# Performance work log

Measured on AMD Instinct MI355X. Metric: run time of the kernel, lower is better.

The kernel has to match this reference:

```python
import jax, jax.numpy as jnp
import numpy as np

# BTT dims for in=out=4096, square mode: m=n=64, a=b=64, rank=8
M, N, A, B_BLK, RANK = 64, 64, 64, 64, 8
OUT_FEATURES = M * A  # 4096


def setup_inputs() -> dict:
    key = jax.random.key(0)
    k_x, k_r, k_l = jax.random.split(key, 3)
    x = jax.random.normal(k_x, (4, 1024, 4096), dtype=jnp.float32)
    # btt_r: (n, b, m*rank); btt_l: (m, rank*n, a)
    btt_r = jax.random.normal(k_r, (N, B_BLK, M * RANK), dtype=jnp.float32) * 0.02
    btt_l = jax.random.normal(k_l, (M, RANK * N, A), dtype=jnp.float32) * 0.02
    bias = jnp.zeros((OUT_FEATURES,), dtype=jnp.float32)
    return {"x": x, "btt_r": btt_r, "btt_l": btt_l, "bias": bias}


def reference(x, btt_r, btt_l, bias):
    n, b, mr = btt_r.shape
    m, rn, a = btt_l.shape
    rank = mr // m
    orig_shape = x.shape
    xr = x.reshape(-1, n, b)          # (B, n, b)
    Bn = xr.shape[0]
    # first contraction: bmm over n blocks -> (n, B, m*rank)
    inner = jnp.einsum('Bnb,nbj->nBj', xr, btt_r)
    # reshape/permute exactly as torch: (n,B,m,r) -> (m,B,n,r) -> (m,B,n*r)
    inner = inner.reshape(n, Bn, m, rank).transpose(2, 1, 0, 3).reshape(m, Bn, rank * n)
    # second contraction: bmm over m blocks -> (B, m, a)
    out = jnp.einsum('mBk,mka->Bma', inner, btt_l)
    out = out.reshape(*orig_shape[:-1], m * a)
    return out + bias
```

## Files before the change

kernel.cpp:

```cpp
#include <hip/hip_runtime.h>


typedef float f32x16 __attribute__((ext_vector_type(16)));
typedef short short8 __attribute__((ext_vector_type(8)));

static __device__ __forceinline__ unsigned short f2b(float f) {
    union { float f; unsigned u; } a; a.f = f;
    unsigned u = a.u;
    unsigned r = u + 0x7fffu + ((u >> 16) & 1u);
    return (unsigned short)(r >> 16);
}

static __device__ __forceinline__ void load_lds_16(const void* gptr, void* lptr) {
    __builtin_amdgcn_global_load_lds(
        (const __attribute__((address_space(1))) unsigned int*)gptr,
        (__attribute__((address_space(3))) unsigned int*)lptr, 16, 0, 0);
}

__global__ __launch_bounds__(256) void prep_all(
    const float* __restrict__ x,
    const float* __restrict__ btt_r,
    const float* __restrict__ btt_l,
    unsigned short* __restrict__ xbt,
    unsigned short* __restrict__ Wtt,
    int nx)
{
    const int tid = threadIdx.x;
    if ((int)blockIdx.x < nx) {
        unsigned i = blockIdx.x * 256 + tid;
        int row = ((i >> 12) << 3) | (i & 7);
        int g   = (i >> 3) & 511;
        float4 v0 = *(const float4*)(x + (size_t)row * 4096 + g * 8);
        float4 v1 = *(const float4*)(x + (size_t)row * 4096 + g * 8 + 4);
        unsigned short o[8];
        o[0] = f2b(v0.x); o[1] = f2b(v0.y); o[2] = f2b(v0.z); o[3] = f2b(v0.w);
        o[4] = f2b(v1.x); o[5] = f2b(v1.y); o[6] = f2b(v1.z); o[7] = f2b(v1.w);
        int ks = g >> 1, half = g & 1;
        int rt = row >> 8, rb = (row >> 5) & 7, l31 = row & 31;
        size_t dst = ((((size_t)rt * 256 + ks) * 8 + rb) * 64 + half * 32 + l31) * 8;
        *(uint4*)(xbt + dst) = *(const uint4*)o;
        return;
    }
    __shared__ float Rs[64][8];
    __shared__ float Ls[8][64];
    const int wb = blockIdx.x - nx;
    const int m = wb >> 6, n = wb & 63;

    if (tid < 128) {
        int b = tid >> 1, rh = (tid & 1) * 4;
        float4 v = *(const float4*)(btt_r + (size_t)n * 32768 + (size_t)b * 512 + m * 8 + rh);
        *(float4*)&Rs[b][rh] = v;
    } else {
        int t2 = (tid - 128) * 4;
        float4 v = *(const float4*)(btt_l + (size_t)m * 32768 + n * 512 + t2);
        *(float4*)&(&Ls[0][0])[t2] = v;
    }
    __syncthreads();

    const int a  = tid >> 2;
    const int bg = (tid & 3) * 16;
    float la[8];
    #pragma unroll
    for (int r = 0; r < 8; ++r) la[r] = Ls[r][a];

    unsigned short o[16];
    #pragma unroll
    for (int bb = 0; bb < 16; ++bb) {
        float acc = 0.f;
        #pragma unroll
        for (int r = 0; r < 8; ++r) acc += Rs[bg + bb][r] * la[r];
        o[bb] = f2b(acc);
    }
    int col = m * 64 + a;
    int ct = col >> 8, rb = (col >> 5) & 7, l31 = col & 31;
    int ks = n * 4 + (bg >> 4);
    size_t dst = ((((size_t)ct * 256 + ks) * 8 + rb) * 64 + l31) * 8;
    *(uint4*)(Wtt + dst)           = *(const uint4*)&o[0];
    *(uint4*)(Wtt + dst + 32 * 8)  = *(const uint4*)&o[8];
}

__global__ __launch_bounds__(512, 2) void gemm_btt(
    const unsigned short* __restrict__ xbt,
    const unsigned short* __restrict__ Wtt,
    const float* __restrict__ bias,
    float* __restrict__ out)
{
    __shared__ unsigned short As[8][4096];
    __shared__ unsigned short Bs[8][4096];

    const int tid = threadIdx.x;
    const int bid = blockIdx.x;
    const int jj = bid >> 3, xc = bid & 7;
    const int rt = (xc >> 1) * 4 + (jj >> 3);
    const int ct = (xc & 1) * 8 + (jj & 7);

    const int wid = tid >> 6, l = tid & 63;
    const int l31 = l & 31, half = l >> 5;
    const int wr = wid >> 2;
    const int wc = wid & 3;

    const unsigned short* xa = xbt + (size_t)rt * (256 * 4096);
    const unsigned short* wa = Wtt + (size_t)ct * (256 * 4096);

    const int offA0 = ((wr * 4 + 0) * 64 + l) * 8;
    const int offA1 = ((wr * 4 + 1) * 64 + l) * 8;
    const int offA2 = ((wr * 4 + 2) * 64 + l) * 8;
    const int offA3 = ((wr * 4 + 3) * 64 + l) * 8;
    const int offB0 = ((wc * 2 + 0) * 64 + l) * 8;
    const int offB1 = ((wc * 2 + 1) * 64 + l) * 8;

    f32x16 acc[4][2];
    #pragma unroll
    for (int i = 0; i < 4; ++i)
        #pragma unroll
        for (int j = 0; j < 2; ++j)
            #pragma unroll
            for (int r = 0; r < 16; ++r)
                acc[i][j][r] = 0.f;

    #define STAGE(s, slot) do {                                               \
        load_lds_16(xa + (size_t)(s) * 4096 + tid * 8, &As[slot][tid * 8]);   \
        load_lds_16(wa + (size_t)(s) * 4096 + tid * 8, &Bs[slot][tid * 8]);   \
    } while (0)

    #define PHASE(slot, STAGE_STMT, VMSTR) do {                               \
        const unsigned short* Ab = &As[slot][0];                              \
        const unsigned short* Bb = &Bs[slot][0];                              \
        short8 af0 = *(const short8*)(Ab + offA0);                            \
        short8 af1 = *(const short8*)(Ab + offA1);                            \
        short8 af2 = *(const short8*)(Ab + offA2);                            \
        short8 af3 = *(const short8*)(Ab + offA3);                            \
        short8 bf0 = *(const short8*)(Bb + offB0);                            \
        short8 bf1 = *(const short8*)(Bb + offB1);                            \
        STAGE_STMT;                                                           \
        asm volatile(VMSTR ::: "memory");                                     \
        __builtin_amdgcn_s_barrier();                                         \
        asm volatile("s_waitcnt lgkmcnt(0)" ::: "memory");                    \
        __builtin_amdgcn_s_setprio(1);                                        \
        acc[0][0] = __builtin_amdgcn_mfma_f32_32x32x16_bf16(af0, bf0, acc[0][0], 0, 0, 0); \
        acc[0][1] = __builtin_amdgcn_mfma_f32_32x32x16_bf16(af0, bf1, acc[0][1], 0, 0, 0); \
        acc[1][0] = __builtin_amdgcn_mfma_f32_32x32x16_bf16(af1, bf0, acc[1][0], 0, 0, 0); \
        acc[1][1] = __builtin_amdgcn_mfma_f32_32x32x16_bf16(af1, bf1, acc[1][1], 0, 0, 0); \
        acc[2][0] = __builtin_amdgcn_mfma_f32_32x32x16_bf16(af2, bf0, acc[2][0], 0, 0, 0); \
        acc[2][1] = __builtin_amdgcn_mfma_f32_32x32x16_bf16(af2, bf1, acc[2][1], 0, 0, 0); \
        acc[3][0] = __builtin_amdgcn_mfma_f32_32x32x16_bf16(af3, bf0, acc[3][0], 0, 0, 0); \
        acc[3][1] = __builtin_amdgcn_mfma_f32_32x32x16_bf16(af3, bf1, acc[3][1], 0, 0, 0); \
        __builtin_amdgcn_s_setprio(0);                                        \
        __builtin_amdgcn_s_barrier();                                         \
        asm volatile("" ::: "memory");                                        \
    } while (0)

    STAGE(0, 0); STAGE(1, 1); STAGE(2, 2); STAGE(3, 3);
    asm volatile("s_waitcnt vmcnt(6)" ::: "memory");
    __builtin_amdgcn_s_barrier();
    asm volatile("" ::: "memory");

    #pragma unroll 1
    for (int it = 0; it < 31; ++it) {
        const int s0 = it * 8;
        PHASE(0, STAGE(s0 + 4,  4), "s_waitcnt vmcnt(6)");
        PHASE(1, STAGE(s0 + 5,  5), "s_waitcnt vmcnt(6)");
        PHASE(2, STAGE(s0 + 6,  6), "s_waitcnt vmcnt(6)");
        PHASE(3, STAGE(s0 + 7,  7), "s_waitcnt vmcnt(6)");
        PHASE(4, STAGE(s0 + 8,  0), "s_waitcnt vmcnt(6)");
        PHASE(5, STAGE(s0 + 9,  1), "s_waitcnt vmcnt(6)");
        PHASE(6, STAGE(s0 + 10, 2), "s_waitcnt vmcnt(6)");
        PHASE(7, STAGE(s0 + 11, 3), "s_waitcnt vmcnt(6)");
    }
    PHASE(0, STAGE(252, 4), "s_waitcnt vmcnt(6)");
    PHASE(1, STAGE(253, 5), "s_waitcnt vmcnt(6)");
    PHASE(2, STAGE(254, 6), "s_waitcnt vmcnt(6)");
    PHASE(3, STAGE(255, 7), "s_waitcnt vmcnt(6)");
    PHASE(4, ((void)0),     "s_waitcnt vmcnt(4)");
    PHASE(5, ((void)0),     "s_waitcnt vmcnt(2)");
    PHASE(6, ((void)0),     "s_waitcnt vmcnt(0)");
    PHASE(7, ((void)0),     "s_waitcnt vmcnt(0)");

    const int rowTileBase = rt * 256 + wr * 128;
    const int colTileBase = ct * 256 + wc * 64;
    #pragma unroll
    for (int jn = 0; jn < 2; ++jn) {
        const int col = colTileBase + jn * 32 + l31;
        const float bv = bias[col];
        #pragma unroll
        for (int i = 0; i < 4; ++i) {
            const int rbase = rowTileBase + i * 32 + 4 * half;
            #pragma unroll
            for (int r = 0; r < 16; ++r) {
                int row = rbase + (r & 3) + 8 * (r >> 2);
                out[(size_t)row * 4096 + col] = acc[i][jn][r] + bv;
            }
        }
    }
    #undef STAGE
    #undef PHASE
}

extern "C" void kernel_launch(void* const* d_in, const int* in_sizes, int n_in,
                              void* d_out, int out_size, void* d_ws, size_t ws_size,
                              hipStream_t stream) {
    const float* x    = (const float*)d_in[0];
    const float* r    = (const float*)d_in[1];
    const float* l    = (const float*)d_in[2];
    const float* bias = (const float*)d_in[3];
    float* out = (float*)d_out;

    unsigned short* xbt = (unsigned short*)d_ws;
    unsigned short* Wtt = (unsigned short*)d_ws + (size_t)4096 * 4096;

    const int rows = in_sizes[0] / 4096;
    const int nx = rows * 4096 / 8 / 256;

    prep_all<<<dim3(nx + 4096), dim3(256), 0, stream>>>(x, r, l, xbt, Wtt, nx);
    gemm_btt<<<dim3((rows / 256) * 16), dim3(512), 0, stream>>>(xbt, Wtt, bias, out);
}
```

Before: 281.8 us.

## Double-buffer LDS fragment registers so reads for the next slot overlap MFMAs

Splits each phase into an LDS read of the next slot into one register set and MFMAs on the previously read set, alternating between two sets of fragment registers. This removes the per-phase lgkmcnt(0) wait before the MFMAs and one of the two barriers per phase, so LDS read latency can be hidden behind matrix math. It costs extra VGPRs for the second fragment set and relies on the compiler to insert correct LDS waits. The single remaining barrier must still keep a slot from being overwritten while other waves are reading it.

```diff
diff --git a/kernel.cpp b/kernel.cpp
--- a/kernel.cpp
+++ b/kernel.cpp
@@ -118,63 +118,73 @@
             for (int r = 0; r < 16; ++r)
                 acc[i][j][r] = 0.f;
 
+    short8 fA0, fA1, fA2, fA3, fB0, fB1;
+    short8 gA0, gA1, gA2, gA3, gB0, gB1;
+
     #define STAGE(s, slot) do {                                               \
         load_lds_16(xa + (size_t)(s) * 4096 + tid * 8, &As[slot][tid * 8]);   \
         load_lds_16(wa + (size_t)(s) * 4096 + tid * 8, &Bs[slot][tid * 8]);   \
     } while (0)
 
-    #define PHASE(slot, STAGE_STMT, VMSTR) do {                               \
+    #define READ6(pA0,pA1,pA2,pA3,pB0,pB1, slot) do {                         \
         const unsigned short* Ab = &As[slot][0];                              \
         const unsigned short* Bb = &Bs[slot][0];                              \
-        short8 af0 = *(const short8*)(Ab + offA0);                            \
-        short8 af1 = *(const short8*)(Ab + offA1);                            \
-        short8 af2 = *(const short8*)(Ab + offA2);                            \
-        short8 af3 = *(const short8*)(Ab + offA3);                            \
-        short8 bf0 = *(const short8*)(Bb + offB0);                            \
-        short8 bf1 = *(const short8*)(Bb + offB1);                            \
+        pA0 = *(const short8*)(Ab + offA0);                                   \
+        pA1 = *(const short8*)(Ab + offA1);                                   \
+        pA2 = *(const short8*)(Ab + offA2);                                   \
+        pA3 = *(const short8*)(Ab + offA3);                                   \
+        pB0 = *(const short8*)(Bb + offB0);                                   \
+        pB1 = *(const short8*)(Bb + offB1);                                   \
+    } while (0)
+
+    #define MFMA8(cA0,cA1,cA2,cA3,cB0,cB1) do {                               \
+        __builtin_amdgcn_s_setprio(1);                                        \
+        acc[0][0] = __builtin_amdgcn_mfma_f32_32x32x16_bf16(cA0, cB0, acc[0][0], 0, 0, 0); \
+        acc[0][1] = __builtin_amdgcn_mfma_f32_32x32x16_bf16(cA0, cB1, acc[0][1], 0, 0, 0); \
+        acc[1][0] = __builtin_amdgcn_mfma_f32_32x32x16_bf16(cA1, cB0, acc[1][0], 0, 0, 0); \
+        acc[1][1] = __builtin_amdgcn_mfma_f32_32x32x16_bf16(cA1, cB1, acc[1][1], 0, 0, 0); \
+        acc[2][0] = __builtin_amdgcn_mfma_f32_32x32x16_bf16(cA2, cB0, acc[2][0], 0, 0, 0); \
+        acc[2][1] = __builtin_amdgcn_mfma_f32_32x32x16_bf16(cA2, cB1, acc[2][1], 0, 0, 0); \
+        acc[3][0] = __builtin_amdgcn_mfma_f32_32x32x16_bf16(cA3, cB0, acc[3][0], 0, 0, 0); \
+        acc[3][1] = __builtin_amdgcn_mfma_f32_32x32x16_bf16(cA3, cB1, acc[3][1], 0, 0, 0); \
+        __builtin_amdgcn_s_setprio(0);                                        \
+    } while (0)
+
+    #define PHASE(STAGE_STMT, VMSTR, rslot, pA0,pA1,pA2,pA3,pB0,pB1, cA0,cA1,cA2,cA3,cB0,cB1) do { \
         STAGE_STMT;                                                           \
         asm volatile(VMSTR ::: "memory");                                     \
         __builtin_amdgcn_s_barrier();                                         \
-        asm volatile("s_waitcnt lgkmcnt(0)" ::: "memory");                    \
-        __builtin_amdgcn_s_setprio(1);                                        \
-        acc[0][0] = __builtin_amdgcn_mfma_f32_32x32x16_bf16(af0, bf0, acc[0][0], 0, 0, 0); \
-        acc[0][1] = __builtin_amdgcn_mfma_f32_32x32x16_bf16(af0, bf1, acc[0][1], 0, 0, 0); \
-        acc[1][0] = __builtin_amdgcn_mfma_f32_32x32x16_bf16(af1, bf0, acc[1][0], 0, 0, 0); \
-        acc[1][1] = __builtin_amdgcn_mfma_f32_32x32x16_bf16(af1, bf1, acc[1][1], 0, 0, 0); \
-        acc[2][0] = __builtin_amdgcn_mfma_f32_32x32x16_bf16(af2, bf0, acc[2][0], 0, 0, 0); \
-        acc[2][1] = __builtin_amdgcn_mfma_f32_32x32x16_bf16(af2, bf1, acc[2][1], 0, 0, 0); \
-        acc[3][0] = __builtin_amdgcn_mfma_f32_32x32x16_bf16(af3, bf0, acc[3][0], 0, 0, 0); \
-        acc[3][1] = __builtin_amdgcn_mfma_f32_32x32x16_bf16(af3, bf1, acc[3][1], 0, 0, 0); \
-        __builtin_amdgcn_s_setprio(0);                                        \
-        __builtin_amdgcn_s_barrier();                                         \
         asm volatile("" ::: "memory");                                        \
+        READ6(pA0,pA1,pA2,pA3,pB0,pB1, rslot);                                \
+        MFMA8(cA0,cA1,cA2,cA3,cB0,cB1);                                       \
     } while (0)
 
     STAGE(0, 0); STAGE(1, 1); STAGE(2, 2); STAGE(3, 3);
     asm volatile("s_waitcnt vmcnt(6)" ::: "memory");
     __builtin_amdgcn_s_barrier();
     asm volatile("" ::: "memory");
+    READ6(fA0, fA1, fA2, fA3, fB0, fB1, 0);
 
     #pragma unroll 1
     for (int it = 0; it < 31; ++it) {
         const int s0 = it * 8;
-        PHASE(0, STAGE(s0 + 4,  4), "s_waitcnt vmcnt(6)");
-        PHASE(1, STAGE(s0 + 5,  5), "s_waitcnt vmcnt(6)");
-        PHASE(2, STAGE(s0 + 6,  6), "s_waitcnt vmcnt(6)");
-        PHASE(3, STAGE(s0 + 7,  7), "s_waitcnt vmcnt(6)");
-        PHASE(4, STAGE(s0 + 8,  0), "s_waitcnt vmcnt(6)");
-        PHASE(5, STAGE(s0 + 9,  1), "s_waitcnt vmcnt(6)");
-        PHASE(6, STAGE(s0 + 10, 2), "s_waitcnt vmcnt(6)");
-        PHASE(7, STAGE(s0 + 11, 3), "s_waitcnt vmcnt(6)");
-    }
-    PHASE(0, STAGE(252, 4), "s_waitcnt vmcnt(6)");
-    PHASE(1, STAGE(253, 5), "s_waitcnt vmcnt(6)");
-    PHASE(2, STAGE(254, 6), "s_waitcnt vmcnt(6)");
-    PHASE(3, STAGE(255, 7), "s_waitcnt vmcnt(6)");
-    PHASE(4, ((void)0),     "s_waitcnt vmcnt(4)");
-    PHASE(5, ((void)0),     "s_waitcnt vmcnt(2)");
-    PHASE(6, ((void)0),     "s_waitcnt vmcnt(0)");
-    PHASE(7, ((void)0),     "s_waitcnt vmcnt(0)");
+        PHASE(STAGE(s0 + 4,  4), "s_waitcnt vmcnt(6)", 1, gA0,gA1,gA2,gA3,gB0,gB1, fA0,fA1,fA2,fA3,fB0,fB1);
+        PHASE(STAGE(s0 + 5,  5), "s_waitcnt vmcnt(6)", 2, fA0,fA1,fA2,fA3,fB0,fB1, gA0,gA1,gA2,gA3,gB0,gB1);
+        PHASE(STAGE(s0 + 6,  6), "s_waitcnt vmcnt(6)", 3, gA0,gA1,gA2,gA3,gB0,gB1, fA0,fA1,fA2,fA3,fB0,fB1);
+        PHASE(STAGE(s0 + 7,  7), "s_waitcnt vmcnt(6)", 4, fA0,fA1,fA2,fA3,fB0,fB1, gA0,gA1,gA2,gA3,gB0,gB1);
+        PHASE(STAGE(s0 + 8,  0), "s_waitcnt vmcnt(6)", 5, gA0,gA1,gA2,gA3,gB0,gB1, fA0,fA1,fA2,fA3,fB0,fB1);
+        PHASE(STAGE(s0 + 9,  1), "s_waitcnt vmcnt(6)", 6, fA0,fA1,fA2,fA3,fB0,fB1, gA0,gA1,gA2,gA3,gB0,gB1);
+        PHASE(STAGE(s0 + 10, 2), "s_waitcnt vmcnt(6)", 7, gA0,gA1,gA2,gA3,gB0,gB1, fA0,fA1,fA2,fA3,fB0,fB1);
+        PHASE(STAGE(s0 + 11, 3), "s_waitcnt vmcnt(6)", 0, fA0,fA1,fA2,fA3,fB0,fB1, gA0,gA1,gA2,gA3,gB0,gB1);
+    }
+    PHASE(STAGE(252, 4), "s_waitcnt vmcnt(6)", 1, gA0,gA1,gA2,gA3,gB0,gB1, fA0,fA1,fA2,fA3,fB0,fB1);
+    PHASE(STAGE(253, 5), "s_waitcnt vmcnt(6)", 2, fA0,fA1,fA2,fA3,fB0,fB1, gA0,gA1,gA2,gA3,gB0,gB1);
+    PHASE(STAGE(254, 6), "s_waitcnt vmcnt(6)", 3, gA0,gA1,gA2,gA3,gB0,gB1, fA0,fA1,fA2,fA3,fB0,fB1);
+    PHASE(STAGE(255, 7), "s_waitcnt vmcnt(6)", 4, fA0,fA1,fA2,fA3,fB0,fB1, gA0,gA1,gA2,gA3,gB0,gB1);
+    PHASE(((void)0),     "s_waitcnt vmcnt(4)", 5, gA0,gA1,gA2,gA3,gB0,gB1, fA0,fA1,fA2,fA3,fB0,fB1);
+    PHASE(((void)0),     "s_waitcnt vmcnt(2)", 6, fA0,fA1,fA2,fA3,fB0,fB1, gA0,gA1,gA2,gA3,gB0,gB1);
+    PHASE(((void)0),     "s_waitcnt vmcnt(0)", 7, gA0,gA1,gA2,gA3,gB0,gB1, fA0,fA1,fA2,fA3,fB0,fB1);
+    MFMA8(gA0, gA1, gA2, gA3, gB0, gB1);
 
     const int rowTileBase = rt * 256 + wr * 128;
     const int colTileBase = ct * 256 + wc * 64;
@@ -193,6 +203,8 @@
         }
     }
     #undef STAGE
+    #undef READ6
+    #undef MFMA8
     #undef PHASE
 }
 
```

Result: no change. 280.5 us (-0.5%).
